# Kernel optimization log

Hardware: AMD Instinct MI355X
Metric: run time of the kernel (lower is better)

Reference implementation:

```python
import jax, jax.numpy as jnp
import numpy as np

B, S, D, T = 512, 65536, 256, 10   # graphs, substructures, emb_dim, num_tasks
THRESHOLD = 0.4                    # CausalGNN threshold default
MEMBER_P = 0.002                   # ~131 substructures per graph


def setup_inputs() -> dict:
    key = jax.random.key(0)
    ks = jax.random.split(key, 8)
    def w(k, shape):
        fan_in = shape[0]
        return jax.random.normal(k, shape, jnp.float32) / np.float32(np.sqrt(fan_in))
    return {
        "h_graph": jax.random.normal(ks[0], (B, D), jnp.float32),
        "h_sub":   jax.random.normal(ks[1], (S, D), jnp.float32),
        "W1": w(ks[2], (D, 2 * D)),  "b1": jnp.zeros((2 * D,), jnp.float32),
        "W2": w(ks[3], (2 * D, 1)),  "b2": jnp.zeros((1,), jnp.float32),
        "Wc": w(ks[4], (2 * D, T)),  "bc": jnp.zeros((T,), jnp.float32),
        # dense [B,S] bool membership: mask[i,j] = substructure j belongs to graph i
        "mask": jax.random.bernoulli(ks[5], MEMBER_P, (B, S)),
    }


def _l2_normalize(x, eps=1e-12):  # F.normalize(p=2, dim=1)
    n = jnp.linalg.norm(x, axis=1, keepdims=True)
    return x / jnp.maximum(n, eps)


def reference(h_graph, h_sub, W1, b1, W2, b2, Wc, bc, mask):
    # SubMaskGenerator: Linear -> ReLU -> Dropout(eval=identity) -> Linear -> sigmoid, squeeze
    gate_logits = (jax.nn.relu(h_sub @ W1 + b1) @ W2 + b2)[:, 0]      # [S]
    subgraph_mask = jax.nn.sigmoid(gate_logits)                        # [S]

    # fused masked segment mean (replaces per-graph python loop + host sync):
    # valid[i,j] = (sub j in graph i) & (gate > threshold)
    valid = mask & (subgraph_mask > THRESHOLD)                         # [B,S] bool
    w = valid.astype(h_sub.dtype)
    counts = w.sum(axis=1, keepdims=True)                              # [B,1]
    sums = w @ h_sub                                                   # [B,D]
    h_sub_aligned = jnp.where(counts > 0, sums / jnp.maximum(counts, 1.0), 0.0)

    h_sub_norm = _l2_normalize(h_sub_aligned)
    h_graph_norm = _l2_normalize(h_graph)
    # F.cosine_similarity(dim=1, eps=1e-8) on the already-normalized vectors
    na = jnp.linalg.norm(h_sub_norm, axis=1)
    ng = jnp.linalg.norm(h_graph_norm, axis=1)
    cos = (h_sub_norm * h_graph_norm).sum(axis=1) / (
        jnp.maximum(na, 1e-8) * jnp.maximum(ng, 1e-8))
    cosine_loss = 1.0 - cos.mean()

    h_combined = jnp.concatenate([h_graph, h_sub_aligned], axis=1)     # [B,2D]
    logits = h_combined @ Wc + bc                                      # [B,T]
    return logits, cosine_loss, subgraph_mask
```

## Files before the change

### kernel.cpp

```cpp
#include <hip/hip_runtime.h>
#include <math.h>

#define D 256
#define H 512
#define TT 10
#define THRESH 0.4f
#define KS 8
#define NSPLIT 8

typedef __attribute__((ext_vector_type(8))) _Float16 half8;
typedef __attribute__((ext_vector_type(4))) float f32x4;

__global__ __launch_bounds__(256) void w1_prep(const float* __restrict__ W1,
                                               short* __restrict__ W1s)
{
    const int tid = blockIdx.x * 256 + threadIdx.x;
    const int lane = tid & 63;
    const int cell = tid >> 6;
    const int k = cell & 7;
    const int n = cell >> 3;
    const int row0 = k * 32 + (lane >> 4) * 8;
    const int col = n * 16 + (lane & 15);
    _Float16 h8[8];
    #pragma unroll
    for (int i = 0; i < 8; ++i)
        h8[i] = (_Float16)W1[(size_t)(row0 + i) * H + col];
    *reinterpret_cast<half8*>(W1s + (((size_t)n * 8 + k) * 64 + lane) * 8) =
        *reinterpret_cast<half8*>(h8);
}

__global__ __launch_bounds__(256, 2) void gate_mfma(
    const float* __restrict__ h_sub,
    const short* __restrict__ W1s,
    const float* __restrict__ b1,
    const float* __restrict__ W2,
    const float* __restrict__ b2,
    float* __restrict__ submask,
    unsigned* __restrict__ gbits)
{
    __shared__ __align__(16) short sW[4][2][4096];
    __shared__ float sb1[H], sw2[H];
    const int tid = threadIdx.x;
    const int lane = tid & 63;
    const int w = tid >> 6;
    const int base = blockIdx.x * 128 + w * 32;
    const int rot = (blockIdx.x * 4 + w) & 31;
    const float bb = b2[0];

    {
        int i = tid * 2;
        *reinterpret_cast<float2*>(&sb1[i]) = *reinterpret_cast<const float2*>(&b1[i]);
        *reinterpret_cast<float2*>(&sw2[i]) = *reinterpret_cast<const float2*>(&W2[i]);
    }

    half8 af[2][KS];
    #pragma unroll
    for (int s = 0; s < 2; ++s) {
        const int row = base + s * 16 + (lane & 15);
        const float* rp = h_sub + (size_t)row * D + (lane >> 4) * 8;
        #pragma unroll
        for (int k = 0; k < KS; ++k) {
            float x[8];
            *reinterpret_cast<float4*>(&x[0]) =
                *reinterpret_cast<const float4*>(rp + k * 32);
            *reinterpret_cast<float4*>(&x[4]) =
                *reinterpret_cast<const float4*>(rp + k * 32 + 4);
            _Float16 h8[8];
            #pragma unroll
            for (int i = 0; i < 8; ++i) h8[i] = (_Float16)x[i];
            af[s][k] = *reinterpret_cast<half8*>(h8);
        }
    }

    __syncthreads();

    auto stage = [&](int c, int b) {
        const char* gp = (const char*)W1s + ((size_t)(c & 31) << 13)
                       + (size_t)lane * 16;
        char* lp0 = (char*)&sW[w][b][0] + lane * 16;
        #pragma unroll
        for (int i = 0; i < 8; ++i) {
            __builtin_amdgcn_global_load_lds(
                (const __attribute__((address_space(1))) void*)(gp + i * 1024),
                (__attribute__((address_space(3))) void*)(lp0 + i * 1024),
                16, 0, 0);
        }
    };

    stage(rot, 0);
    stage(rot + 1, 1);

    float lp[2][4] = {{0.f,0.f,0.f,0.f},{0.f,0.f,0.f,0.f}};

    for (int cc = 0; cc < 32; ++cc) {
        if (cc < 31) asm volatile("s_waitcnt vmcnt(8)" ::: "memory");
        else         asm volatile("s_waitcnt vmcnt(0)" ::: "memory");
        __builtin_amdgcn_sched_barrier(0);

        const int c = (cc + rot) & 31;
        const short* buf = &sW[w][cc & 1][0];
        f32x4 acc[2];
        acc[0] = (f32x4){0.f,0.f,0.f,0.f};
        acc[1] = (f32x4){0.f,0.f,0.f,0.f};

        #pragma unroll
        for (int k = 0; k < KS; ++k) {
            half8 bh = *reinterpret_cast<const half8*>(buf + (k * 64 + lane) * 8);
            acc[0] = __builtin_amdgcn_mfma_f32_16x16x32_f16(af[0][k], bh, acc[0], 0, 0, 0);
            acc[1] = __builtin_amdgcn_mfma_f32_16x16x32_f16(af[1][k], bh, acc[1], 0, 0, 0);
        }

        const int h = c * 16 + (lane & 15);
        const float b1h = sb1[h], w2h = sw2[h];
        #pragma unroll
        for (int s = 0; s < 2; ++s)
            #pragma unroll
            for (int j = 0; j < 4; ++j) {
                float v = acc[s][j] + b1h;
                v = v > 0.f ? v : 0.f;
                lp[s][j] = fmaf(v, w2h, lp[s][j]);
            }

        __builtin_amdgcn_sched_barrier(0);
        if (cc < 30) stage(cc + rot + 2, cc & 1);
    }

    #pragma unroll
    for (int m = 1; m < 16; m <<= 1)
        #pragma unroll
        for (int s = 0; s < 2; ++s)
            #pragma unroll
            for (int j = 0; j < 4; ++j)
                lp[s][j] += __shfl_xor(lp[s][j], m);

    const int g = lane >> 4;
    unsigned bits = 0;
    float sig[2][4];
    #pragma unroll
    for (int s = 0; s < 2; ++s)
        #pragma unroll
        for (int j = 0; j < 4; ++j) {
            sig[s][j] = 1.f / (1.f + expf(-(lp[s][j] + bb)));
            if (sig[s][j] > THRESH) bits |= 1u << (s * 16 + g * 4 + j);
        }
    bits |= __shfl_xor(bits, 16);
    bits |= __shfl_xor(bits, 32);
    if (lane == 0) gbits[blockIdx.x * 4 + w] = bits;

    if ((lane & 15) == 0)
        #pragma unroll
        for (int s = 0; s < 2; ++s)
            #pragma unroll
            for (int j = 0; j < 4; ++j)
                submask[base + s * 16 + g * 4 + j] = sig[s][j];
}

__global__ __launch_bounds__(256) void seg_scan(
    const float* __restrict__ h_sub,
    const int*   __restrict__ mask,
    const unsigned* __restrict__ gbits,
    float* __restrict__ psum,
    int*   __restrict__ pcnt,
    int S)
{
    const int i = blockIdx.x / NSPLIT;
    const int p = blockIdx.x % NSPLIT;
    const int tid = threadIdx.x;
    const int lane = tid & 63;
    const int w = tid >> 6;
    const int seg = S / NSPLIT;
    const int start = p * seg;
    const int* mrow = mask + (size_t)i * S + start;

    __shared__ unsigned sbits[8192 / 32];
    {
        const int nw = seg / 32;
        for (int t = tid; t < nw; t += 256) sbits[t] = gbits[(start >> 5) + t];
    }
    __syncthreads();

    float4 acc = make_float4(0.f, 0.f, 0.f, 0.f);
    int cnt = 0;

    const int per = seg / 4;
    for (int base = w * per; base < (w + 1) * per; base += 256) {
        const int j0 = base + (lane << 2);
        int4 m4 = *reinterpret_cast<const int4*>(mrow + j0);
        const unsigned bw = sbits[j0 >> 5];
        const int sh = j0 & 31;
        unsigned long long bal[4];
        bal[0] = __ballot((m4.x != 0) & ((bw >> (sh + 0)) & 1u));
        bal[1] = __ballot((m4.y != 0) & ((bw >> (sh + 1)) & 1u));
        bal[2] = __ballot((m4.z != 0) & ((bw >> (sh + 2)) & 1u));
        bal[3] = __ballot((m4.w != 0) & ((bw >> (sh + 3)) & 1u));
        #pragma unroll
        for (int s = 0; s < 4; ++s) {
            unsigned long long b = bal[s];
            while (b) {
                int t = __builtin_ctzll(b);
                b &= b - 1;
                int jj = start + base + (t << 2) + s;
                float4 hv = *reinterpret_cast<const float4*>(
                    h_sub + (size_t)jj * D + (lane << 2));
                acc.x += hv.x; acc.y += hv.y; acc.z += hv.z; acc.w += hv.w;
                cnt++;
            }
        }
    }

    __shared__ float ssum[4][D];
    __shared__ int   scnt[4];
    *reinterpret_cast<float4*>(&ssum[w][lane << 2]) = acc;
    if (lane == 0) scnt[w] = cnt;
    __syncthreads();

    float a = ssum[0][tid] + ssum[1][tid] + ssum[2][tid] + ssum[3][tid];
    psum[(size_t)blockIdx.x * D + tid] = a;
    if (tid == 0) pcnt[blockIdx.x] = scnt[0] + scnt[1] + scnt[2] + scnt[3];
}

__global__ __launch_bounds__(256) void seg_combine(
    const float* __restrict__ h_graph,
    const float* __restrict__ psum,
    const int*   __restrict__ pcnt,
    const float* __restrict__ Wc,
    const float* __restrict__ bc,
    float* __restrict__ logits,
    float* __restrict__ cos_ws)
{
    const int i = blockIdx.x;
    const int tid = threadIdx.x;
    const int lane = tid & 63;
    const int w = tid >> 6;

    float a = 0.f;
    int c = 0;
    #pragma unroll
    for (int p = 0; p < NSPLIT; ++p) {
        a += psum[((size_t)i * NSPLIT + p) * D + tid];
        c += pcnt[i * NSPLIT + p];
    }
    a = (c > 0) ? (a / (float)c) : 0.f;
    const float g = h_graph[(size_t)i * D + tid];

    float r0 = a * a, r1 = g * g, r2 = a * g;
    #pragma unroll
    for (int m = 1; m < 64; m <<= 1) {
        r0 += __shfl_xor(r0, m);
        r1 += __shfl_xor(r1, m);
        r2 += __shfl_xor(r2, m);
    }
    __shared__ float red[4][3];
    if (lane == 0) { red[w][0] = r0; red[w][1] = r1; red[w][2] = r2; }
    __syncthreads();
    if (tid == 0) {
        float a2 = red[0][0] + red[1][0] + red[2][0] + red[3][0];
        float g2 = red[0][1] + red[1][1] + red[2][1] + red[3][1];
        float ag = red[0][2] + red[1][2] + red[2][2] + red[3][2];
        float an = sqrtf(a2), gn = sqrtf(g2);
        float cs = (c > 0) ? (ag / (fmaxf(an, 1e-12f) * fmaxf(gn, 1e-12f))) : 0.f;
        cos_ws[i] = cs;
    }

    float lg[TT];
    #pragma unroll
    for (int t = 0; t < TT; ++t)
        lg[t] = g * Wc[(size_t)tid * TT + t] + a * Wc[(size_t)(D + tid) * TT + t];
    #pragma unroll
    for (int m = 1; m < 64; m <<= 1)
        #pragma unroll
        for (int t = 0; t < TT; ++t) lg[t] += __shfl_xor(lg[t], m);
    __shared__ float lpart[4][TT];
    if (lane == 0)
        #pragma unroll
        for (int t = 0; t < TT; ++t) lpart[w][t] = lg[t];
    __syncthreads();
    if (tid < TT)
        logits[(size_t)i * TT + tid] =
            lpart[0][tid] + lpart[1][tid] + lpart[2][tid] + lpart[3][tid] + bc[tid];
}

__global__ void loss_kernel(const float* __restrict__ cos_ws,
                            float* __restrict__ out, int B)
{
    const int lane = threadIdx.x;
    float s = 0.f;
    for (int i = lane; i < B; i += 64) s += cos_ws[i];
    #pragma unroll
    for (int m = 1; m < 64; m <<= 1) s += __shfl_xor(s, m);
    if (lane == 0) out[0] = 1.0f - s / (float)B;
}

extern "C" void kernel_launch(void* const* d_in, const int* in_sizes, int n_in,
                              void* d_out, int out_size, void* d_ws, size_t ws_size,
                              hipStream_t stream)
{
    const float* h_graph = (const float*)d_in[0];
    const float* h_sub   = (const float*)d_in[1];
    const float* W1      = (const float*)d_in[2];
    const float* b1      = (const float*)d_in[3];
    const float* W2      = (const float*)d_in[4];
    const float* b2      = (const float*)d_in[5];
    const float* Wc      = (const float*)d_in[6];
    const float* bc      = (const float*)d_in[7];
    const int*   mask    = (const int*)d_in[8];

    const int B = in_sizes[0] / D;
    const int S = in_sizes[1] / D;

    float* out     = (float*)d_out;
    float* logits  = out;
    float* loss    = out + (size_t)B * TT;
    float* submask = loss + 1;

    char* ws = (char*)d_ws;
    short*    W1s    = (short*)ws;
    unsigned* gbits  = (unsigned*)(ws + 512 * 1024);
    int*      pcnt   = (int*)(ws + 528 * 1024);
    float*    cos_ws = (float*)(ws + 560 * 1024);
    float*    psum   = (float*)(ws + 1024 * 1024);

    w1_prep<<<64, 256, 0, stream>>>(W1, W1s);
    gate_mfma<<<S / 128, 256, 0, stream>>>(h_sub, W1s, b1, W2, b2, submask, gbits);
    seg_scan<<<B * NSPLIT, 256, 0, stream>>>(h_sub, mask, gbits, psum, pcnt, S);
    seg_combine<<<B, 256, 0, stream>>>(h_graph, psum, pcnt, Wc, bc, logits, cos_ws);
    loss_kernel<<<1, 64, 0, stream>>>(cos_ws, loss, B);
}
```

Before: 77.33 us.

## Compress membership mask to bitmasks inside gate kernel using extra waves

The gate kernel now launches 512 threads per block. Four extra waves, running alongside the MFMA gate computation, read the dense int mask and ballot it into 64-bit membership bitmasks. The segment scan then reads these compact bitmasks instead of the 128 MB int mask, and NSPLIT doubles to 16 for more parallelism in the scan. The aim is to overlap the mask stream with the compute-bound gate and shrink the scan's traffic. The cost is an extra bitmask write and read, plus a larger block that may lower occupancy.

```diff
diff --git a/kernel.cpp b/kernel.cpp
--- a/kernel.cpp
+++ b/kernel.cpp
@@ -6,7 +6,7 @@
 #define TT 10
 #define THRESH 0.4f
 #define KS 8
-#define NSPLIT 8
+#define NSPLIT 16
 
 typedef __attribute__((ext_vector_type(8))) _Float16 half8;
 typedef __attribute__((ext_vector_type(4))) float f32x4;
@@ -29,135 +29,163 @@
         *reinterpret_cast<half8*>(h8);
 }
 
-__global__ __launch_bounds__(256, 2) void gate_mfma(
+__global__ __launch_bounds__(512, 4) void gate_fused(
     const float* __restrict__ h_sub,
     const short* __restrict__ W1s,
     const float* __restrict__ b1,
     const float* __restrict__ W2,
     const float* __restrict__ b2,
+    const int*   __restrict__ mask,
     float* __restrict__ submask,
-    unsigned* __restrict__ gbits)
+    unsigned* __restrict__ gbits,
+    unsigned long long* __restrict__ cmask)
 {
     __shared__ __align__(16) short sW[4][2][4096];
     __shared__ float sb1[H], sw2[H];
     const int tid = threadIdx.x;
     const int lane = tid & 63;
     const int w = tid >> 6;
+    const bool isGate = (w < 4);
+    const float bb = b2[0];
+
     const int base = blockIdx.x * 128 + w * 32;
     const int rot = (blockIdx.x * 4 + w) & 31;
-    const float bb = b2[0];
-
-    {
+
+    half8 af[2][KS];
+
+    if (isGate) {
         int i = tid * 2;
         *reinterpret_cast<float2*>(&sb1[i]) = *reinterpret_cast<const float2*>(&b1[i]);
         *reinterpret_cast<float2*>(&sw2[i]) = *reinterpret_cast<const float2*>(&W2[i]);
-    }
-
-    half8 af[2][KS];
-    #pragma unroll
-    for (int s = 0; s < 2; ++s) {
-        const int row = base + s * 16 + (lane & 15);
-        const float* rp = h_sub + (size_t)row * D + (lane >> 4) * 8;
-        #pragma unroll
-        for (int k = 0; k < KS; ++k) {
-            float x[8];
-            *reinterpret_cast<float4*>(&x[0]) =
-                *reinterpret_cast<const float4*>(rp + k * 32);
-            *reinterpret_cast<float4*>(&x[4]) =
-                *reinterpret_cast<const float4*>(rp + k * 32 + 4);
-            _Float16 h8[8];
-            #pragma unroll
-            for (int i = 0; i < 8; ++i) h8[i] = (_Float16)x[i];
-            af[s][k] = *reinterpret_cast<half8*>(h8);
+
+        #pragma unroll
+        for (int s = 0; s < 2; ++s) {
+            const int row = base + s * 16 + (lane & 15);
+            const float* rp = h_sub + (size_t)row * D + (lane >> 4) * 8;
+            #pragma unroll
+            for (int k = 0; k < KS; ++k) {
+                float x[8];
+                *reinterpret_cast<float4*>(&x[0]) =
+                    *reinterpret_cast<const float4*>(rp + k * 32);
+                *reinterpret_cast<float4*>(&x[4]) =
+                    *reinterpret_cast<const float4*>(rp + k * 32 + 4);
+                _Float16 h8[8];
+                #pragma unroll
+                for (int i2 = 0; i2 < 8; ++i2) h8[i2] = (_Float16)x[i2];
+                af[s][k] = *reinterpret_cast<half8*>(h8);
+            }
         }
     }
 
     __syncthreads();
 
-    auto stage = [&](int c, int b) {
-        const char* gp = (const char*)W1s + ((size_t)(c & 31) << 13)
-                       + (size_t)lane * 16;
-        char* lp0 = (char*)&sW[w][b][0] + lane * 16;
-        #pragma unroll
-        for (int i = 0; i < 8; ++i) {
-            __builtin_amdgcn_global_load_lds(
-                (const __attribute__((address_space(1))) void*)(gp + i * 1024),
-                (__attribute__((address_space(3))) void*)(lp0 + i * 1024),
-                16, 0, 0);
+    if (isGate) {
+        auto stage = [&](int c, int b) {
+            const char* gp = (const char*)W1s + ((size_t)(c & 31) << 13)
+                           + (size_t)lane * 16;
+            char* lp0 = (char*)&sW[w][b][0] + lane * 16;
+            #pragma unroll
+            for (int i = 0; i < 8; ++i) {
+                __builtin_amdgcn_global_load_lds(
+                    (const __attribute__((address_space(1))) void*)(gp + i * 1024),
+                    (__attribute__((address_space(3))) void*)(lp0 + i * 1024),
+                    16, 0, 0);
+            }
+        };
+
+        stage(rot, 0);
+        stage(rot + 1, 1);
+
+        float lp[2][4] = {{0.f,0.f,0.f,0.f},{0.f,0.f,0.f,0.f}};
+
+        for (int cc = 0; cc < 32; ++cc) {
+            if (cc < 31) asm volatile("s_waitcnt vmcnt(8)" ::: "memory");
+            else         asm volatile("s_waitcnt vmcnt(0)" ::: "memory");
+            __builtin_amdgcn_sched_barrier(0);
+
+            const int c = (cc + rot) & 31;
+            const short* buf = &sW[w][cc & 1][0];
+            f32x4 acc[2];
+            acc[0] = (f32x4){0.f,0.f,0.f,0.f};
+            acc[1] = (f32x4){0.f,0.f,0.f,0.f};
+
+            #pragma unroll
+            for (int k = 0; k < KS; ++k) {
+                half8 bh = *reinterpret_cast<const half8*>(buf + (k * 64 + lane) * 8);
+                acc[0] = __builtin_amdgcn_mfma_f32_16x16x32_f16(af[0][k], bh, acc[0], 0, 0, 0);
+                acc[1] = __builtin_amdgcn_mfma_f32_16x16x32_f16(af[1][k], bh, acc[1], 0, 0, 0);
+            }
+
+            const int h = c * 16 + (lane & 15);
+            const float b1h = sb1[h], w2h = sw2[h];
+            #pragma unroll
+            for (int s = 0; s < 2; ++s)
+                #pragma unroll
+                for (int j = 0; j < 4; ++j) {
+                    float v = acc[s][j] + b1h;
+                    v = v > 0.f ? v : 0.f;
+                    lp[s][j] = fmaf(v, w2h, lp[s][j]);
+                }
+
+            __builtin_amdgcn_sched_barrier(0);
+            if (cc < 30) stage(cc + rot + 2, cc & 1);
         }
-    };
-
-    stage(rot, 0);
-    stage(rot + 1, 1);
-
-    float lp[2][4] = {{0.f,0.f,0.f,0.f},{0.f,0.f,0.f,0.f}};
-
-    for (int cc = 0; cc < 32; ++cc) {
-        if (cc < 31) asm volatile("s_waitcnt vmcnt(8)" ::: "memory");
-        else         asm volatile("s_waitcnt vmcnt(0)" ::: "memory");
-        __builtin_amdgcn_sched_barrier(0);
-
-        const int c = (cc + rot) & 31;
-        const short* buf = &sW[w][cc & 1][0];
-        f32x4 acc[2];
-        acc[0] = (f32x4){0.f,0.f,0.f,0.f};
-        acc[1] = (f32x4){0.f,0.f,0.f,0.f};
-
-        #pragma unroll
-        for (int k = 0; k < KS; ++k) {
-            half8 bh = *reinterpret_cast<const half8*>(buf + (k * 64 + lane) * 8);
-            acc[0] = __builtin_amdgcn_mfma_f32_16x16x32_f16(af[0][k], bh, acc[0], 0, 0, 0);
-            acc[1] = __builtin_amdgcn_mfma_f32_16x16x32_f16(af[1][k], bh, acc[1], 0, 0, 0);
+
+        #pragma unroll
+        for (int m = 1; m < 16; m <<= 1)
+            #pragma unroll
+            for (int s = 0; s < 2; ++s)
+                #pragma unroll
+                for (int j = 0; j < 4; ++j)
+                    lp[s][j] += __shfl_xor(lp[s][j], m);
+
+        const int g = lane >> 4;
+        unsigned bits = 0;
+        float sig[2][4];
+        #pragma unroll
+        for (int s = 0; s < 2; ++s)
+            #pragma unroll
+            for (int j = 0; j < 4; ++j) {
+                sig[s][j] = 1.f / (1.f + expf(-(lp[s][j] + bb)));
+                if (sig[s][j] > THRESH) bits |= 1u << (s * 16 + g * 4 + j);
+            }
+        bits |= __shfl_xor(bits, 16);
+        bits |= __shfl_xor(bits, 32);
+        if (lane == 0) gbits[blockIdx.x * 4 + w] = bits;
+
+        if ((lane & 15) == 0)
+            #pragma unroll
+            for (int s = 0; s < 2; ++s)
+                #pragma unroll
+                for (int j = 0; j < 4; ++j)
+                    submask[base + s * 16 + g * 4 + j] = sig[s][j];
+    } else {
+        const int mw = blockIdx.x * 4 + (w - 4);
+        const size_t g0 = (size_t)mw * 64;
+        for (int it = 0; it < 8; ++it) {
+            int4 m4[8];
+            #pragma unroll
+            for (int u = 0; u < 8; ++u)
+                m4[u] = *reinterpret_cast<const int4*>(
+                    mask + (g0 + it * 8 + u) * 256 + (lane << 2));
+            #pragma unroll
+            for (int u = 0; u < 8; ++u) {
+                unsigned long long c0 = __ballot(m4[u].x != 0);
+                unsigned long long c1 = __ballot(m4[u].y != 0);
+                unsigned long long c2 = __ballot(m4[u].z != 0);
+                unsigned long long c3 = __ballot(m4[u].w != 0);
+                if (lane == 0) {
+                    unsigned long long* cp = cmask + (g0 + it * 8 + u) * 4;
+                    cp[0] = c0; cp[1] = c1; cp[2] = c2; cp[3] = c3;
+                }
+            }
         }
-
-        const int h = c * 16 + (lane & 15);
-        const float b1h = sb1[h], w2h = sw2[h];
-        #pragma unroll
-        for (int s = 0; s < 2; ++s)
-            #pragma unroll
-            for (int j = 0; j < 4; ++j) {
-                float v = acc[s][j] + b1h;
-                v = v > 0.f ? v : 0.f;
-                lp[s][j] = fmaf(v, w2h, lp[s][j]);
-            }
-
-        __builtin_amdgcn_sched_barrier(0);
-        if (cc < 30) stage(cc + rot + 2, cc & 1);
-    }
-
-    #pragma unroll
-    for (int m = 1; m < 16; m <<= 1)
-        #pragma unroll
-        for (int s = 0; s < 2; ++s)
-            #pragma unroll
-            for (int j = 0; j < 4; ++j)
-                lp[s][j] += __shfl_xor(lp[s][j], m);
-
-    const int g = lane >> 4;
-    unsigned bits = 0;
-    float sig[2][4];
-    #pragma unroll
-    for (int s = 0; s < 2; ++s)
-        #pragma unroll
-        for (int j = 0; j < 4; ++j) {
-            sig[s][j] = 1.f / (1.f + expf(-(lp[s][j] + bb)));
-            if (sig[s][j] > THRESH) bits |= 1u << (s * 16 + g * 4 + j);
-        }
-    bits |= __shfl_xor(bits, 16);
-    bits |= __shfl_xor(bits, 32);
-    if (lane == 0) gbits[blockIdx.x * 4 + w] = bits;
-
-    if ((lane & 15) == 0)
-        #pragma unroll
-        for (int s = 0; s < 2; ++s)
-            #pragma unroll
-            for (int j = 0; j < 4; ++j)
-                submask[base + s * 16 + g * 4 + j] = sig[s][j];
+    }
 }
 
 __global__ __launch_bounds__(256) void seg_scan(
     const float* __restrict__ h_sub,
-    const int*   __restrict__ mask,
+    const unsigned long long* __restrict__ cmask,
     const unsigned* __restrict__ gbits,
     float* __restrict__ psum,
     int*   __restrict__ pcnt,
@@ -170,36 +198,34 @@
     const int w = tid >> 6;
     const int seg = S / NSPLIT;
     const int start = p * seg;
-    const int* mrow = mask + (size_t)i * S + start;
-
-    __shared__ unsigned sbits[8192 / 32];
-    {
-        const int nw = seg / 32;
-        for (int t = tid; t < nw; t += 256) sbits[t] = gbits[(start >> 5) + t];
-    }
+    const unsigned long long* cm =
+        cmask + ((size_t)i * (S / 256) + (size_t)p * (seg / 256)) * 4;
+
+    __shared__ unsigned sbits[4096 / 32];
+    if (tid < seg / 32) sbits[tid] = gbits[(start >> 5) + tid];
     __syncthreads();
 
     float4 acc = make_float4(0.f, 0.f, 0.f, 0.f);
     int cnt = 0;
 
-    const int per = seg / 4;
-    for (int base = w * per; base < (w + 1) * per; base += 256) {
-        const int j0 = base + (lane << 2);
-        int4 m4 = *reinterpret_cast<const int4*>(mrow + j0);
+    #pragma unroll
+    for (int it = 0; it < 4; ++it) {
+        const int g = w * 4 + it;
+        const int j0 = g * 256 + (lane << 2);
         const unsigned bw = sbits[j0 >> 5];
         const int sh = j0 & 31;
         unsigned long long bal[4];
-        bal[0] = __ballot((m4.x != 0) & ((bw >> (sh + 0)) & 1u));
-        bal[1] = __ballot((m4.y != 0) & ((bw >> (sh + 1)) & 1u));
-        bal[2] = __ballot((m4.z != 0) & ((bw >> (sh + 2)) & 1u));
-        bal[3] = __ballot((m4.w != 0) & ((bw >> (sh + 3)) & 1u));
+        bal[0] = __ballot((bw >> (sh + 0)) & 1u) & cm[(size_t)g * 4 + 0];
+        bal[1] = __ballot((bw >> (sh + 1)) & 1u) & cm[(size_t)g * 4 + 1];
+        bal[2] = __ballot((bw >> (sh + 2)) & 1u) & cm[(size_t)g * 4 + 2];
+        bal[3] = __ballot((bw >> (sh + 3)) & 1u) & cm[(size_t)g * 4 + 3];
         #pragma unroll
         for (int s = 0; s < 4; ++s) {
             unsigned long long b = bal[s];
             while (b) {
                 int t = __builtin_ctzll(b);
                 b &= b - 1;
-                int jj = start + base + (t << 2) + s;
+                int jj = start + g * 256 + (t << 2) + s;
                 float4 hv = *reinterpret_cast<const float4*>(
                     h_sub + (size_t)jj * D + (lane << 2));
                 acc.x += hv.x; acc.y += hv.y; acc.z += hv.z; acc.w += hv.w;
@@ -317,12 +343,15 @@
     short*    W1s    = (short*)ws;
     unsigned* gbits  = (unsigned*)(ws + 512 * 1024);
     int*      pcnt   = (int*)(ws + 528 * 1024);
-    float*    cos_ws = (float*)(ws + 560 * 1024);
+    float*    cos_ws = (float*)(ws + 576 * 1024);
     float*    psum   = (float*)(ws + 1024 * 1024);
+    unsigned long long* cmask =
+        (unsigned long long*)(ws + 16 * 1024 * 1024);
 
     w1_prep<<<64, 256, 0, stream>>>(W1, W1s);
-    gate_mfma<<<S / 128, 256, 0, stream>>>(h_sub, W1s, b1, W2, b2, submask, gbits);
-    seg_scan<<<B * NSPLIT, 256, 0, stream>>>(h_sub, mask, gbits, psum, pcnt, S);
+    gate_fused<<<S / 128, 512, 0, stream>>>(
+        h_sub, W1s, b1, W2, b2, mask, submask, gbits, cmask);
+    seg_scan<<<B * NSPLIT, 256, 0, stream>>>(h_sub, cmask, gbits, psum, pcnt, S);
     seg_combine<<<B, 256, 0, stream>>>(h_graph, psum, pcnt, Wc, bc, logits, cos_ws);
     loss_kernel<<<1, 64, 0, stream>>>(cos_ws, loss, B);
 }
```

Measured after the change: 78.13 us. About the same (+1.0%).

## Share W1 tiles across waves in gate kernel and widen seg_scan split

Applied to the files above, without the earlier changes.

The gate kernel now stages 64-column W1 chunks into one block-shared double buffer, cooperatively loaded by all four waves with block barriers, instead of each wave streaming its own 16-column tiles. Each wave issues eight MFMAs per k-step with raised priority. This cuts redundant global and LDS traffic for W1 but adds barrier synchronization. seg_scan doubles NSPLIT to 16 and preloads all mask vectors up front for more memory-level parallelism and more blocks, at the cost of more partial sums for the combine step.

```diff
diff --git a/kernel.cpp b/kernel.cpp
--- a/kernel.cpp
+++ b/kernel.cpp
@@ -6,7 +6,7 @@
 #define TT 10
 #define THRESH 0.4f
 #define KS 8
-#define NSPLIT 8
+#define NSPLIT 16
 
 typedef __attribute__((ext_vector_type(8))) _Float16 half8;
 typedef __attribute__((ext_vector_type(4))) float f32x4;
@@ -38,13 +38,13 @@
     float* __restrict__ submask,
     unsigned* __restrict__ gbits)
 {
-    __shared__ __align__(16) short sW[4][2][4096];
+    __shared__ __align__(16) short sB[2][16384];
     __shared__ float sb1[H], sw2[H];
     const int tid = threadIdx.x;
     const int lane = tid & 63;
     const int w = tid >> 6;
     const int base = blockIdx.x * 128 + w * 32;
-    const int rot = (blockIdx.x * 4 + w) & 31;
+    const int rot = blockIdx.x & 7;
     const float bb = b2[0];
 
     {
@@ -74,55 +74,75 @@
 
     __syncthreads();
 
-    auto stage = [&](int c, int b) {
-        const char* gp = (const char*)W1s + ((size_t)(c & 31) << 13)
-                       + (size_t)lane * 16;
-        char* lp0 = (char*)&sW[w][b][0] + lane * 16;
+    auto stage = [&](int cc, int b) {
+        const int c = (cc + rot) & 7;
+        const char* gp = (const char*)W1s + ((size_t)c << 15) + (size_t)tid * 16;
+        char* lp0 = (char*)&sB[b][0] + (size_t)tid * 16;
         #pragma unroll
         for (int i = 0; i < 8; ++i) {
             __builtin_amdgcn_global_load_lds(
-                (const __attribute__((address_space(1))) void*)(gp + i * 1024),
-                (__attribute__((address_space(3))) void*)(lp0 + i * 1024),
+                (const __attribute__((address_space(1))) void*)(gp + i * 4096),
+                (__attribute__((address_space(3))) void*)(lp0 + i * 4096),
                 16, 0, 0);
         }
     };
 
-    stage(rot, 0);
-    stage(rot + 1, 1);
+    stage(0, 0);
+    stage(1, 1);
 
     float lp[2][4] = {{0.f,0.f,0.f,0.f},{0.f,0.f,0.f,0.f}};
 
-    for (int cc = 0; cc < 32; ++cc) {
-        if (cc < 31) asm volatile("s_waitcnt vmcnt(8)" ::: "memory");
-        else         asm volatile("s_waitcnt vmcnt(0)" ::: "memory");
+    for (int cc = 0; cc < 8; ++cc) {
+        if (cc < 7) asm volatile("s_waitcnt vmcnt(8)" ::: "memory");
+        else        asm volatile("s_waitcnt vmcnt(0)" ::: "memory");
+        __builtin_amdgcn_s_barrier();
         __builtin_amdgcn_sched_barrier(0);
 
-        const int c = (cc + rot) & 31;
-        const short* buf = &sW[w][cc & 1][0];
-        f32x4 acc[2];
-        acc[0] = (f32x4){0.f,0.f,0.f,0.f};
-        acc[1] = (f32x4){0.f,0.f,0.f,0.f};
-
+        const short* buf = &sB[cc & 1][0];
+        const int c = (cc + rot) & 7;
+
+        f32x4 acc[2][4];
+        #pragma unroll
+        for (int s = 0; s < 2; ++s)
+            #pragma unroll
+            for (int nt = 0; nt < 4; ++nt)
+                acc[s][nt] = (f32x4){0.f,0.f,0.f,0.f};
+
+        __builtin_amdgcn_s_setprio(1);
         #pragma unroll
         for (int k = 0; k < KS; ++k) {
-            half8 bh = *reinterpret_cast<const half8*>(buf + (k * 64 + lane) * 8);
-            acc[0] = __builtin_amdgcn_mfma_f32_16x16x32_f16(af[0][k], bh, acc[0], 0, 0, 0);
-            acc[1] = __builtin_amdgcn_mfma_f32_16x16x32_f16(af[1][k], bh, acc[1], 0, 0, 0);
-        }
-
-        const int h = c * 16 + (lane & 15);
-        const float b1h = sb1[h], w2h = sw2[h];
-        #pragma unroll
-        for (int s = 0; s < 2; ++s)
-            #pragma unroll
-            for (int j = 0; j < 4; ++j) {
-                float v = acc[s][j] + b1h;
-                v = v > 0.f ? v : 0.f;
-                lp[s][j] = fmaf(v, w2h, lp[s][j]);
-            }
+            half8 bh0 = *reinterpret_cast<const half8*>(buf + ((0 * 8 + k) * 64 + lane) * 8);
+            half8 bh1 = *reinterpret_cast<const half8*>(buf + ((1 * 8 + k) * 64 + lane) * 8);
+            half8 bh2 = *reinterpret_cast<const half8*>(buf + ((2 * 8 + k) * 64 + lane) * 8);
+            half8 bh3 = *reinterpret_cast<const half8*>(buf + ((3 * 8 + k) * 64 + lane) * 8);
+            acc[0][0] = __builtin_amdgcn_mfma_f32_16x16x32_f16(af[0][k], bh0, acc[0][0], 0, 0, 0);
+            acc[1][0] = __builtin_amdgcn_mfma_f32_16x16x32_f16(af[1][k], bh0, acc[1][0], 0, 0, 0);
+            acc[0][1] = __builtin_amdgcn_mfma_f32_16x16x32_f16(af[0][k], bh1, acc[0][1], 0, 0, 0);
+            acc[1][1] = __builtin_amdgcn_mfma_f32_16x16x32_f16(af[1][k], bh1, acc[1][1], 0, 0, 0);
+            acc[0][2] = __builtin_amdgcn_mfma_f32_16x16x32_f16(af[0][k], bh2, acc[0][2], 0, 0, 0);
+            acc[1][2] = __builtin_amdgcn_mfma_f32_16x16x32_f16(af[1][k], bh2, acc[1][2], 0, 0, 0);
+            acc[0][3] = __builtin_amdgcn_mfma_f32_16x16x32_f16(af[0][k], bh3, acc[0][3], 0, 0, 0);
+            acc[1][3] = __builtin_amdgcn_mfma_f32_16x16x32_f16(af[1][k], bh3, acc[1][3], 0, 0, 0);
+        }
+        __builtin_amdgcn_s_setprio(0);
+
+        #pragma unroll
+        for (int nt = 0; nt < 4; ++nt) {
+            const int hc = c * 64 + nt * 16 + (lane & 15);
+            const float b1h = sb1[hc], w2h = sw2[hc];
+            #pragma unroll
+            for (int s = 0; s < 2; ++s)
+                #pragma unroll
+                for (int j = 0; j < 4; ++j) {
+                    float v = acc[s][nt][j] + b1h;
+                    v = v > 0.f ? v : 0.f;
+                    lp[s][j] = fmaf(v, w2h, lp[s][j]);
+                }
+        }
 
         __builtin_amdgcn_sched_barrier(0);
-        if (cc < 30) stage(cc + rot + 2, cc & 1);
+        __builtin_amdgcn_s_barrier();
+        if (cc < 6) stage(cc + 2, cc & 1);
     }
 
     #pragma unroll
@@ -172,34 +192,37 @@
     const int start = p * seg;
     const int* mrow = mask + (size_t)i * S + start;
 
-    __shared__ unsigned sbits[8192 / 32];
-    {
-        const int nw = seg / 32;
-        for (int t = tid; t < nw; t += 256) sbits[t] = gbits[(start >> 5) + t];
-    }
+    __shared__ unsigned sbits[4096 / 32];
+    if (tid < seg / 32) sbits[tid] = gbits[(start >> 5) + tid];
+
+    const int wbase = w * 1024;
+    int4 m4[4];
+    #pragma unroll
+    for (int it = 0; it < 4; ++it)
+        m4[it] = *reinterpret_cast<const int4*>(mrow + wbase + it * 256 + (lane << 2));
+
     __syncthreads();
 
     float4 acc = make_float4(0.f, 0.f, 0.f, 0.f);
     int cnt = 0;
 
-    const int per = seg / 4;
-    for (int base = w * per; base < (w + 1) * per; base += 256) {
-        const int j0 = base + (lane << 2);
-        int4 m4 = *reinterpret_cast<const int4*>(mrow + j0);
+    #pragma unroll
+    for (int it = 0; it < 4; ++it) {
+        const int j0 = wbase + it * 256 + (lane << 2);
         const unsigned bw = sbits[j0 >> 5];
         const int sh = j0 & 31;
         unsigned long long bal[4];
-        bal[0] = __ballot((m4.x != 0) & ((bw >> (sh + 0)) & 1u));
-        bal[1] = __ballot((m4.y != 0) & ((bw >> (sh + 1)) & 1u));
-        bal[2] = __ballot((m4.z != 0) & ((bw >> (sh + 2)) & 1u));
-        bal[3] = __ballot((m4.w != 0) & ((bw >> (sh + 3)) & 1u));
+        bal[0] = __ballot((m4[it].x != 0) & ((bw >> (sh + 0)) & 1u));
+        bal[1] = __ballot((m4[it].y != 0) & ((bw >> (sh + 1)) & 1u));
+        bal[2] = __ballot((m4[it].z != 0) & ((bw >> (sh + 2)) & 1u));
+        bal[3] = __ballot((m4[it].w != 0) & ((bw >> (sh + 3)) & 1u));
         #pragma unroll
         for (int s = 0; s < 4; ++s) {
             unsigned long long b = bal[s];
             while (b) {
                 int t = __builtin_ctzll(b);
                 b &= b - 1;
-                int jj = start + base + (t << 2) + s;
+                int jj = start + wbase + it * 256 + (t << 2) + s;
                 float4 hv = *reinterpret_cast<const float4*>(
                     h_sub + (size_t)jj * D + (lane << 2));
                 acc.x += hv.x; acc.y += hv.y; acc.z += hv.z; acc.w += hv.w;
@@ -317,7 +340,7 @@
     short*    W1s    = (short*)ws;
     unsigned* gbits  = (unsigned*)(ws + 512 * 1024);
     int*      pcnt   = (int*)(ws + 528 * 1024);
-    float*    cos_ws = (float*)(ws + 560 * 1024);
+    float*    cos_ws = (float*)(ws + 576 * 1024);
     float*    psum   = (float*)(ws + 1024 * 1024);
 
     w1_prep<<<64, 256, 0, stream>>>(W1, W1s);
```

Result: faster. 71.66 us (-7.3%).
